# Performance work log

Hardware: AMD Instinct MI355X
Metric: run time of the kernel (lower is better)

The kernel has to match this reference:

```python
import jax, jax.numpy as jnp
import numpy as np

B, T, D = 8, 512, 512
MAX_DUR = 15          # durations drawn from [0,16) then clamped to >=1
MAX_LEN = T * MAX_DUR # static padded frame length (torch pads to per-batch max)


def setup_inputs() -> dict:
    key = jax.random.key(0)
    kf, kd = jax.random.split(key)
    features = jax.random.normal(kf, (B, T, D), dtype=jnp.float32)
    durations = jax.random.randint(kd, (B, T), 0, 16, dtype=jnp.int32)
    return {"features": features, "durations": durations}


def reference(features, durations):
    """Duration-based length regulation (variable-length expand + pad).

    For each batch b, phoneme t is repeated durations[b,t] times along the
    frame axis; sequences are zero-padded to MAX_LEN. Implemented as a
    vectorized cumsum + searchsorted gather (no per-element host syncs).
    """
    Bv, Tv, Dv = features.shape
    dur = jnp.maximum(durations, 1)               # clamp(min=1) as in forward()
    cum = jnp.cumsum(dur, axis=1)                 # (B, T) exclusive-right frame boundaries
    pos = jnp.arange(MAX_LEN, dtype=cum.dtype)    # (MAX_LEN,)
    # idx[b, n] = source phoneme for output frame n: count of boundaries <= n
    idx = jax.vmap(lambda c: jnp.searchsorted(c, pos, side="right"))(cum)  # (B, MAX_LEN)
    valid = pos[None, :] < cum[:, -1:]            # (B, MAX_LEN) frames within total length
    idx = jnp.minimum(idx, Tv - 1)                # keep gather in-bounds for padded frames
    out = jnp.take_along_axis(features, idx[..., None], axis=1)  # (B, MAX_LEN, D)
    return jnp.where(valid[..., None], out, jnp.zeros((), features.dtype))
```

## Files before the change

kernel.cpp:

```cpp
#include <hip/hip_runtime.h>

#define BB 8
#define TT 512
#define DD 512
#define MAX_LEN 7680
#define PPB 4
#define BPB (TT / PPB)
#define QPB (PPB * 15)
#define QPS (QPB / 2)

__global__ __launch_bounds__(256) void regulate_kernel(
    const float4* __restrict__ feat,
    const int*    __restrict__ dur,
    float4*       __restrict__ out)
{
    const int t    = threadIdx.x;
    const int blk  = blockIdx.x & (BPB - 1);
    const int b    = blockIdx.x >> 7;
    const int lane = t & 127;
    const int sub  = t >> 7;
    const int l    = t & 63;

    const int4* d4p = (const int4*)(dur + b * TT + 8 * l);
    int4 da = d4p[0];
    int4 db = d4p[1];

    const int ph_a = PPB * blk + 2 * sub;
    const float4* featb = feat + (size_t)b * TT * (DD / 4) + lane;
    float4 va = featb[(size_t)ph_a * (DD / 4)];
    float4 vb = featb[(size_t)(ph_a + 1) * (DD / 4)];

    int d[8] = {da.x, da.y, da.z, da.w, db.x, db.y, db.z, db.w};
    int s[8];
    int run = 0;
#pragma unroll
    for (int i = 0; i < 8; ++i) {
        int di = d[i] < 1 ? 1 : d[i];
        run += di;
        s[i] = run;
    }
    int incl = run;
#pragma unroll
    for (int off = 1; off < 64; off <<= 1) {
        int v = __shfl_up(incl, off, 64);
        if (l >= off) incl += v;
    }
    const int pre = incl - run;

    const int L = blk >> 1;
    int sm1, sa0, sa1, sa2, sa3;
    if (blk & 1) {
        sm1 = __shfl(s[3], L, 64);
        sa0 = __shfl(s[4], L, 64); sa1 = __shfl(s[5], L, 64);
        sa2 = __shfl(s[6], L, 64); sa3 = __shfl(s[7], L, 64);
    } else {
        sm1 = 0;
        sa0 = __shfl(s[0], L, 64); sa1 = __shfl(s[1], L, 64);
        sa2 = __shfl(s[2], L, 64); sa3 = __shfl(s[3], L, 64);
    }
    const int preL  = __shfl(pre, L, 64);
    const int total = __shfl(incl, 63, 64);

    const int st0 = preL + sm1;
    const int d0 = sa0 - sm1, d1 = sa1 - sa0, d2 = sa2 - sa1, d3 = sa3 - sa2;
    const int sum01 = d0 + d1;
    const int sum23 = d2 + d3;

    const int P = total + QPB * blk - st0;

    int start, na, nb, z0, zn;
    if (sub == 0) { start = st0;          na = d0; nb = d1; z0 = P;                  zn = QPS - sum01; }
    else          { start = st0 + sum01;  na = d2; nb = d3; z0 = P + (QPS - sum01);  zn = QPS - sum23; }

    float4* outb = out + (size_t)b * MAX_LEN * (DD / 4) + lane;
    size_t p = (size_t)start * (DD / 4);
    for (int k = 0; k < na; ++k) { outb[p] = va; p += DD / 4; }
    for (int k = 0; k < nb; ++k) { outb[p] = vb; p += DD / 4; }

    const float4 zero = make_float4(0.f, 0.f, 0.f, 0.f);
    p = (size_t)z0 * (DD / 4);
    for (int k = 0; k < zn; ++k) { outb[p] = zero; p += DD / 4; }
}

extern "C" void kernel_launch(void* const* d_in, const int* in_sizes, int n_in,
                              void* d_out, int out_size, void* d_ws, size_t ws_size,
                              hipStream_t stream) {
    const float* feat;
    const int*   dur;
    if (in_sizes[0] == BB * TT) {
        dur  = (const int*)d_in[0];
        feat = (const float*)d_in[1];
    } else {
        feat = (const float*)d_in[0];
        dur  = (const int*)d_in[1];
    }
    float* out = (float*)d_out;

    regulate_kernel<<<BB * BPB, 256, 0, stream>>>(
        (const float4*)feat, dur, (float4*)out);
}
```

Baseline: 130.8 us.

## Halve phonemes per block and unroll fixed-count store loop merging data and zero rows

```diff
diff --git a/kernel.cpp b/kernel.cpp
--- a/kernel.cpp
+++ b/kernel.cpp
@@ -4,10 +4,10 @@
 #define TT 512
 #define DD 512
 #define MAX_LEN 7680
-#define PPB 4
+#define PPB 2
 #define BPB (TT / PPB)
 #define QPB (PPB * 15)
-#define QPS (QPB / 2)
+#define QPS 15
 
 __global__ __launch_bounds__(256) void regulate_kernel(
     const float4* __restrict__ feat,
@@ -16,7 +16,7 @@
 {
     const int t    = threadIdx.x;
     const int blk  = blockIdx.x & (BPB - 1);
-    const int b    = blockIdx.x >> 7;
+    const int b    = blockIdx.x >> 8;
     const int lane = t & 127;
     const int sub  = t >> 7;
     const int l    = t & 63;
@@ -25,10 +25,9 @@
     int4 da = d4p[0];
     int4 db = d4p[1];
 
-    const int ph_a = PPB * blk + 2 * sub;
+    const int ph = PPB * blk + sub;
     const float4* featb = feat + (size_t)b * TT * (DD / 4) + lane;
-    float4 va = featb[(size_t)ph_a * (DD / 4)];
-    float4 vb = featb[(size_t)(ph_a + 1) * (DD / 4)];
+    float4 v = featb[(size_t)ph * (DD / 4)];
 
     int d[8] = {da.x, da.y, da.z, da.w, db.x, db.y, db.z, db.w};
     int s[8];
@@ -42,44 +41,45 @@
     int incl = run;
 #pragma unroll
     for (int off = 1; off < 64; off <<= 1) {
-        int v = __shfl_up(incl, off, 64);
-        if (l >= off) incl += v;
+        int vv = __shfl_up(incl, off, 64);
+        if (l >= off) incl += vv;
     }
     const int pre = incl - run;
 
-    const int L = blk >> 1;
-    int sm1, sa0, sa1, sa2, sa3;
-    if (blk & 1) {
-        sm1 = __shfl(s[3], L, 64);
-        sa0 = __shfl(s[4], L, 64); sa1 = __shfl(s[5], L, 64);
-        sa2 = __shfl(s[6], L, 64); sa3 = __shfl(s[7], L, 64);
-    } else {
-        sm1 = 0;
-        sa0 = __shfl(s[0], L, 64); sa1 = __shfl(s[1], L, 64);
-        sa2 = __shfl(s[2], L, 64); sa3 = __shfl(s[3], L, 64);
-    }
+    const int L  = blk >> 2;
+    const int jj = blk & 3;
+    int t0 = __shfl(s[0], L, 64), t1 = __shfl(s[1], L, 64),
+        t2 = __shfl(s[2], L, 64), t3 = __shfl(s[3], L, 64),
+        t4 = __shfl(s[4], L, 64), t5 = __shfl(s[5], L, 64),
+        t6 = __shfl(s[6], L, 64), t7 = __shfl(s[7], L, 64);
+    int tm1, ta, tb;
+    if      (jj == 0) { tm1 = 0;  ta = t0; tb = t1; }
+    else if (jj == 1) { tm1 = t1; ta = t2; tb = t3; }
+    else if (jj == 2) { tm1 = t3; ta = t4; tb = t5; }
+    else              { tm1 = t5; ta = t6; tb = t7; }
+
     const int preL  = __shfl(pre, L, 64);
     const int total = __shfl(incl, 63, 64);
 
-    const int st0 = preL + sm1;
-    const int d0 = sa0 - sm1, d1 = sa1 - sa0, d2 = sa2 - sa1, d3 = sa3 - sa2;
-    const int sum01 = d0 + d1;
-    const int sum23 = d2 + d3;
+    const int st0 = preL + tm1;
+    const int d0  = ta - tm1;
+    const int d1  = tb - ta;
 
     const int P = total + QPB * blk - st0;
 
-    int start, na, nb, z0, zn;
-    if (sub == 0) { start = st0;          na = d0; nb = d1; z0 = P;                  zn = QPS - sum01; }
-    else          { start = st0 + sum01;  na = d2; nb = d3; z0 = P + (QPS - sum01);  zn = QPS - sum23; }
+    int start, n, z0;
+    if (sub == 0) { start = st0;      n = d0; z0 = P; }
+    else          { start = st0 + d0; n = d1; z0 = P + (QPS - d0); }
 
     float4* outb = out + (size_t)b * MAX_LEN * (DD / 4) + lane;
-    size_t p = (size_t)start * (DD / 4);
-    for (int k = 0; k < na; ++k) { outb[p] = va; p += DD / 4; }
-    for (int k = 0; k < nb; ++k) { outb[p] = vb; p += DD / 4; }
-
     const float4 zero = make_float4(0.f, 0.f, 0.f, 0.f);
-    p = (size_t)z0 * (DD / 4);
-    for (int k = 0; k < zn; ++k) { outb[p] = zero; p += DD / 4; }
+#pragma unroll
+    for (int k = 0; k < QPS; ++k) {
+        const bool real = k < n;
+        const int  row  = real ? (start + k) : (z0 + (k - n));
+        const float4 w  = real ? v : zero;
+        outb[(size_t)row * (DD / 4)] = w;
+    }
 }
 
 extern "C" void kernel_launch(void* const* d_in, const int* in_sizes, int n_in,
```

New measurement: 132.2 us. Within noise of the previous version (+1.1%).
